# Optimization experiments

Hardware: AMD Instinct MI355X
Metric: run time of the kernel (lower is better)

The kernel has to match this reference:

```python
import jax, jax.numpy as jnp
import numpy as np

B, D, T, H, K = 16, 1024, 1024, 1024, 2  # batch, in_channels, seq_len, hidden_size, kernel_size


def setup_inputs() -> dict:
    key = jax.random.key(0)
    k1, k2, k3 = jax.random.split(key, 3)
    inputs = jax.random.normal(k1, (B, D, T), dtype=jnp.float32)
    # Conv1D kernel in OIH layout: [3H, D, K]; scaled to keep gates in a sane range
    conv_w = jax.random.normal(k2, (3 * H, D, K), dtype=jnp.float32) / np.float32(np.sqrt(D * K))
    conv_b = jax.random.normal(k3, (3 * H,), dtype=jnp.float32) * 0.01
    return {"inputs": inputs, "conv_w": conv_w, "conv_b": conv_b}


def reference(inputs, conv_w, conv_b):
    # inputs: [B, D, T] (channels_first, as in the keras call signature)
    # Causal conv: left-pad time by K-1, then VALID conv -> [B, 3H, T]
    padded = jnp.pad(inputs, ((0, 0), (0, 0), (K - 1, 0)))
    gates = jax.lax.conv_general_dilated(
        padded, conv_w, window_strides=(1,), padding="VALID",
        dimension_numbers=("NCH", "OIH", "NCH"))
    gates = gates + conv_b[None, :, None]
    gates = jnp.transpose(gates, (0, 2, 1))  # [B, T, 3H]
    z = jnp.tanh(gates[..., :H])
    f = jax.nn.sigmoid(gates[..., H:2 * H])
    o = jax.nn.sigmoid(gates[..., 2 * H:])

    # fo-pooling linear recurrence: c_t = f_t * c_{t-1} + (1 - f_t) * z_t, c_0 = 0
    zf = (jnp.transpose(z, (1, 0, 2)), jnp.transpose(f, (1, 0, 2)))  # time-major [T, B, H]

    def step(c, zf_t):
        z_t, f_t = zf_t
        c_new = f_t * c + (1.0 - f_t) * z_t
        return c_new, c_new

    c0 = jnp.zeros((B, H), dtype=inputs.dtype)
    _, c_seq = jax.lax.scan(step, c0, zf)
    c_seq = jnp.transpose(c_seq, (1, 0, 2))  # [B, T, H]
    h_seq = o * c_seq
    return c_seq, h_seq
```

## Files before the change

### kernel.cpp

```cpp
#include <hip/hip_runtime.h>

#define Bsz 16
#define Dch 1024
#define Tsz 1024
#define Hsz 1024
#define Mtot (Bsz*Tsz)
#define K2   (2*Dch)
#define Ntot (3*Hsz)
#define NCH  32
#define CL   32
#define NT   32

typedef __attribute__((ext_vector_type(8))) short bf16x8;
typedef __attribute__((ext_vector_type(4))) float f32x4;

__device__ __forceinline__ unsigned short f2bf(float x) {
    unsigned u = __float_as_uint(x);
    u += 0x7FFFu + ((u >> 16) & 1u);
    return (unsigned short)(u >> 16);
}
__device__ __forceinline__ float bf2f(unsigned short s) {
    return __uint_as_float(((unsigned)s) << 16);
}

#define GLOAD_LDS16(gp, lp) \
    __builtin_amdgcn_global_load_lds((const __attribute__((address_space(1))) void*)(gp), \
                                     (__attribute__((address_space(3))) void*)(lp), 16, 0, 0)

#define LDSB(p) ((unsigned)(unsigned long long)(__attribute__((address_space(3))) const void*)(p))

#define DSR(dst, addr, off) \
    asm volatile("ds_read_b128 %0, %1 offset:" #off : "=v"(dst) : "v"(addr))

#define WAITLG(n) do { \
    asm volatile("s_waitcnt lgkmcnt(" #n ")" ::: "memory"); \
    __builtin_amdgcn_sched_barrier(0); } while (0)

#define VMC(n) do { \
    asm volatile("s_waitcnt vmcnt(" #n ")" ::: "memory"); \
    __builtin_amdgcn_sched_barrier(0); } while (0)

#define BAR __builtin_amdgcn_s_barrier()

__global__ __launch_bounds__(256)
void prep(const float* __restrict__ x, unsigned short* __restrict__ a2,
          const float* __restrict__ w, unsigned short* __restrict__ wb) {
    __shared__ float Xs[64][66];
    int bid = blockIdx.x;
    int tid = threadIdx.x;
    if (bid >= 4096) {
        int i0 = (bid - 4096) * 256 + tid;
        #pragma unroll
        for (int k = 0; k < 4; k++) {
            int i = i0 + k * (1536 * 256);
            float4 v = ((const float4*)w)[i];
            ushort4 r;
            r.x = f2bf(v.x); r.y = f2bf(v.y); r.z = f2bf(v.z); r.w = f2bf(v.w);
            ((ushort4*)wb)[i] = r;
        }
        return;
    }
    int b   = bid >> 8;
    int tt0 = ((bid >> 4) & 15) << 6;
    int dd0 = (bid & 15) << 6;
    int colt = tid & 63, rowq = tid >> 6;
    const size_t xbase = (size_t)b * (Dch * Tsz);
    #pragma unroll
    for (int r = 0; r < 16; r++) {
        int dd = r * 4 + rowq;
        Xs[dd][1 + colt] = x[xbase + (size_t)(dd0 + dd) * Tsz + tt0 + colt];
    }
    if (tid < 64) {
        Xs[tid][0] = (tt0 == 0) ? 0.f : x[xbase + (size_t)(dd0 + tid) * Tsz + tt0 - 1];
    }
    __syncthreads();
    #pragma unroll
    for (int r = 0; r < 16; r++) {
        int tr = r * 4 + rowq;
        int dc = colt;
        float v0 = Xs[dc][tr];
        float v1 = Xs[dc][tr + 1];
        unsigned pack = (unsigned)f2bf(v0) | ((unsigned)f2bf(v1) << 16);
        int m = (b << 10) + tt0 + tr;
        ((unsigned*)a2)[(size_t)m * (K2 / 2) + dd0 + dc] = pack;
    }
}

#define MF(slot, bset, p) do { \
    _Pragma("unroll") for (int ks_ = 0; ks_ < 2; ++ks_) { \
      _Pragma("unroll") for (int d_ = 0; d_ < 2; ++d_) { \
        _Pragma("unroll") for (int j_ = 0; j_ < 4; ++j_) { \
          acc[2*(p)+d_][j_] = __builtin_amdgcn_mfma_f32_16x16x32_bf16( \
              slot[d_][ks_], bset[ks_][j_], acc[2*(p)+d_][j_], 0, 0, 0); \
        } } } } while (0)

__global__ __launch_bounds__(512, 2)
void gemm_gates(const unsigned short* __restrict__ A, const unsigned short* __restrict__ Bt,
                const float* __restrict__ bias,
                float* __restrict__ zc, float* __restrict__ fh, unsigned short* __restrict__ ob) {
    __shared__ __align__(16) unsigned short As[2][16384];
    __shared__ __align__(16) unsigned short Bs[2][16384];

    int tid  = threadIdx.x;
    int wv   = tid >> 6, lane = tid & 63;
    int wm   = wv >> 2, wn = wv & 3;
    int lm   = lane & 15, q = lane >> 4;

    int bid = blockIdx.x;
    int swz = (bid & 7) * 96 + (bid >> 3);
    int mt = swz / 12, nt = swz % 12;
    int m0 = mt << 8, n0 = nt << 8;

    const unsigned short* Abase = A  + (size_t)m0 * K2;
    const unsigned short* Bbase = Bt + (size_t)n0 * K2;

    int loff   = (wv * 8 + (lane >> 3)) * K2 + (((lane & 7) ^ (lane >> 3)) << 3);
    int ldsoff = wv * 8 * 64;

    int sw  = lm & 7;
    int kc0 = (q ^ sw) << 3;
    int kc1 = ((4 + q) ^ sw) << 3;
    int aoff = (wm * 128 + lm) * 64;
    int boff = (wn * 64 + lm) * 64;

    unsigned asb = LDSB(&As[0][0]);
    unsigned bsb = LDSB(&Bs[0][0]);
    unsigned aA0 = asb + (unsigned)(aoff + kc0) * 2u;
    unsigned aA1 = asb + (unsigned)(aoff + kc1) * 2u;
    unsigned aB0 = bsb + (unsigned)(boff + kc0) * 2u;
    unsigned aB1 = bsb + (unsigned)(boff + kc1) * 2u;

    f32x4 acc[8][4] = {};
    bf16x8 afA[2][2], afB[2][2];
    bf16x8 bfrE[2][4], bfrO[2][4];

#define STAGE_A(t, h) do { \
    const unsigned short* g_ = Abase + (h) * (128 * K2) + (t) * 64 + loff; \
    unsigned short* l_ = &As[(t) & 1][(h) * 8192 + ldsoff]; \
    GLOAD_LDS16(g_, l_); \
    GLOAD_LDS16(g_ + 64 * K2, l_ + 64 * 64); } while (0)
#define STAGE_B(t, h) do { \
    const unsigned short* g_ = Bbase + (h) * (128 * K2) + (t) * 64 + loff; \
    unsigned short* l_ = &Bs[(t) & 1][(h) * 8192 + ldsoff]; \
    GLOAD_LDS16(g_, l_); \
    GLOAD_LDS16(g_ + 64 * K2, l_ + 64 * 64); } while (0)

#define R_AFP(slot, o0, o1, bo) do { \
    DSR(slot[0][0], aA0 + (bo), o0); DSR(slot[0][1], aA1 + (bo), o0); \
    DSR(slot[1][0], aA0 + (bo), o1); DSR(slot[1][1], aA1 + (bo), o1); } while (0)
#define R_BH0(set, bo) do { \
    DSR(set[0][0], aB0 + (bo), 0);    DSR(set[1][0], aB1 + (bo), 0); \
    DSR(set[0][1], aB0 + (bo), 2048); DSR(set[1][1], aB1 + (bo), 2048); } while (0)
#define R_BH1(set, bo) do { \
    DSR(set[0][2], aB0 + (bo), 4096); DSR(set[1][2], aB1 + (bo), 4096); \
    DSR(set[0][3], aB0 + (bo), 6144); DSR(set[1][3], aB1 + (bo), 6144); } while (0)

#define PRIO1 __builtin_amdgcn_s_setprio(1)
#define PRIO0 do { __builtin_amdgcn_s_setprio(0); __builtin_amdgcn_sched_barrier(0); } while (0)

#define PH0(T, CB, BC) do { \
    R_AFP(afB, 4096, 6144, CB); \
    STAGE_A((T) + 1, 1); \
    WAITLG(4); \
    PRIO1; MF(afA, BC, 0); PRIO0; } while (0)
#define PH1(T, CB, NB, BC, BN) do { \
    R_AFP(afA, 8192, 10240, CB); \
    R_BH0(BN, NB); \
    STAGE_A((T) + 1, 0); \
    WAITLG(8); \
    PRIO1; MF(afB, BC, 1); PRIO0; } while (0)
#define PH2(T, CB, NB, BC, BN) do { \
    R_AFP(afB, 12288, 14336, CB); \
    R_BH1(BN, NB); \
    STAGE_B((T) + 2, 1); \
    WAITLG(8); \
    PRIO1; MF(afA, BC, 2); PRIO0; } while (0)
#define PH3(T, NB, BC) do { \
    R_AFP(afA, 0, 2048, NB); \
    STAGE_B((T) + 2, 0); \
    WAITLG(4); \
    PRIO1; MF(afB, BC, 3); PRIO0; } while (0)

    STAGE_A(0, 0); STAGE_A(0, 1); STAGE_B(0, 0); STAGE_B(0, 1);
    STAGE_B(1, 1); STAGE_B(1, 0);
    VMC(4); BAR;
    R_AFP(afA, 0, 2048, 0u);
    R_BH0(bfrE, 0u); R_BH1(bfrE, 0u);
    __builtin_amdgcn_sched_barrier(0);

    #pragma unroll 1
    for (int tp = 0; tp < 15; ++tp) {
        int t0 = 2 * tp;
        PH0(t0, 0u, bfrE);                 VMC(2); BAR;
        PH1(t0, 0u, 32768u, bfrE, bfrO);           BAR;
        PH2(t0, 0u, 32768u, bfrE, bfrO);   VMC(2); BAR;
        PH3(t0, 32768u, bfrE);                     BAR;
        PH0(t0 + 1, 32768u, bfrO);         VMC(2); BAR;
        PH1(t0 + 1, 32768u, 0u, bfrO, bfrE);       BAR;
        PH2(t0 + 1, 32768u, 0u, bfrO, bfrE); VMC(2); BAR;
        PH3(t0 + 1, 0u, bfrO);                     BAR;
    }

    PH0(30, 0u, bfrE);                     VMC(2); BAR;
    PH1(30, 0u, 32768u, bfrE, bfrO);               BAR;
    R_AFP(afB, 12288, 14336, 0u);
    R_BH1(bfrO, 32768u);
    WAITLG(8);
    PRIO1; MF(afA, bfrE, 2); PRIO0;
    VMC(0); BAR;
    R_AFP(afA, 0, 2048, 32768u);
    WAITLG(4);
    PRIO1; MF(afB, bfrE, 3); PRIO0;
    BAR;

    R_AFP(afB, 4096, 6144, 32768u);
    WAITLG(4);
    PRIO1; MF(afA, bfrO, 0); PRIO0; BAR;
    R_AFP(afA, 8192, 10240, 32768u);
    WAITLG(4);
    PRIO1; MF(afB, bfrO, 1); PRIO0; BAR;
    R_AFP(afB, 12288, 14336, 32768u);
    WAITLG(4);
    PRIO1; MF(afA, bfrO, 2); PRIO0; BAR;
    WAITLG(0);
    PRIO1; MF(afB, bfrO, 3); PRIO0;

    int gt = nt >> 2;
    #pragma unroll
    for (int i = 0; i < 8; ++i) {
        int mrow = m0 + wm * 128 + i * 16 + q * 4;
        #pragma unroll
        for (int j = 0; j < 4; ++j) {
            int n = n0 + wn * 64 + j * 16 + lm;
            float bv = bias[n];
            int hcol = n & 1023;
            #pragma unroll
            for (int r = 0; r < 4; ++r) {
                float g = acc[i][j][r] + bv;
                size_t idx = (size_t)(mrow + r) * Hsz + hcol;
                if (gt == 0) {
                    float e = __expf(2.f * g);
                    zc[idx] = __fdividef(e - 1.f, e + 1.f);
                } else {
                    float s = __fdividef(1.f, 1.f + __expf(-g));
                    if (gt == 1) fh[idx] = s;
                    else         ob[idx] = f2bf(s);
                }
            }
        }
    }
}

__global__ __launch_bounds__(256)
void scan1(const float* __restrict__ zc, const float* __restrict__ fh,
           float* __restrict__ Aw, float* __restrict__ Bw) {
    int blk = blockIdx.x;
    int hb = blk & 1, ch = (blk >> 1) & 31, b = blk >> 6;
    int h = hb * 512 + threadIdx.x * 2;
    size_t base = ((size_t)b << 20) + ((size_t)(ch * CL) << 10) + h;
    float ax = 1.f, ay = 1.f, bx = 0.f, by = 0.f;
    #pragma unroll 8
    for (int s = 0; s < CL; s++) {
        size_t idx = base + ((size_t)s << 10);
        float2 z = *(const float2*)&zc[idx];
        float2 f = *(const float2*)&fh[idx];
        ax *= f.x; ay *= f.y;
        bx = z.x + f.x * (bx - z.x);
        by = z.y + f.y * (by - z.y);
    }
    int o = (ch * Bsz + b) * Hsz + h;
    *(float2*)&Aw[o] = make_float2(ax, ay);
    *(float2*)&Bw[o] = make_float2(bx, by);
}

__global__ __launch_bounds__(256)
void scan3(float* __restrict__ zc, float* __restrict__ fh,
           const unsigned short* __restrict__ ob,
           const float* __restrict__ Aw, const float* __restrict__ Bw) {
    int blk = blockIdx.x;
    int hb = blk & 1, ch = (blk >> 1) & 31, b = blk >> 6;
    int h = hb * 512 + threadIdx.x * 2;
    float cx = 0.f, cy = 0.f;
    for (int cp = 0; cp < ch; cp++) {
        int o = (cp * Bsz + b) * Hsz + h;
        float2 A = *(const float2*)&Aw[o];
        float2 B = *(const float2*)&Bw[o];
        cx = A.x * cx + B.x;
        cy = A.y * cy + B.y;
    }
    size_t base = ((size_t)b << 20) + ((size_t)(ch * CL) << 10) + h;
    #pragma unroll 8
    for (int s = 0; s < CL; s++) {
        size_t idx = base + ((size_t)s << 10);
        float2 z = *(const float2*)&zc[idx];
        float2 f = *(const float2*)&fh[idx];
        unsigned ov = *(const unsigned*)&ob[idx];
        cx = z.x + f.x * (cx - z.x);
        cy = z.y + f.y * (cy - z.y);
        *(float2*)&zc[idx] = make_float2(cx, cy);
        float ox = bf2f((unsigned short)(ov & 0xFFFF));
        float oy = bf2f((unsigned short)(ov >> 16));
        *(float2*)&fh[idx] = make_float2(ox * cx, oy * cy);
    }
}

extern "C" void kernel_launch(void* const* d_in, const int* in_sizes, int n_in,
                              void* d_out, int out_size, void* d_ws, size_t ws_size,
                              hipStream_t stream) {
    const float* x    = (const float*)d_in[0];
    const float* w    = (const float*)d_in[1];
    const float* bias = (const float*)d_in[2];
    float* zc = (float*)d_out;
    float* fh = (float*)d_out + (size_t)Mtot * Hsz;
    unsigned short* a2 = (unsigned short*)d_ws;
    unsigned short* wb = a2 + (size_t)Mtot * K2;
    unsigned short* ob = wb + (size_t)Ntot * K2;
    float* Aw = (float*)(ob + (size_t)Mtot * Hsz);
    float* Bw = Aw + NCH * Bsz * Hsz;

    hipLaunchKernelGGL(prep, dim3(5632), dim3(256), 0, stream, x, a2, w, wb);
    hipLaunchKernelGGL(gemm_gates, dim3(768), dim3(512), 0, stream, a2, wb, bias, zc, fh, ob);
    hipLaunchKernelGGL(scan1, dim3(1024), dim3(256), 0, stream, zc, fh, Aw, Bw);
    hipLaunchKernelGGL(scan3, dim3(1024), dim3(256), 0, stream, zc, fh, ob, Aw, Bw);
}
```

Measured before the change: 453.8 us.

## Restructure GEMM pipeline to stage full tiles once per iteration with fewer barriers

```diff
diff --git a/kernel.cpp b/kernel.cpp
--- a/kernel.cpp
+++ b/kernel.cpp
@@ -158,72 +158,56 @@
 #define PRIO1 __builtin_amdgcn_s_setprio(1)
 #define PRIO0 do { __builtin_amdgcn_s_setprio(0); __builtin_amdgcn_sched_barrier(0); } while (0)
 
-#define PH0(T, CB, BC) do { \
+#define PH012(CB, BC) do { \
     R_AFP(afB, 4096, 6144, CB); \
-    STAGE_A((T) + 1, 1); \
     WAITLG(4); \
-    PRIO1; MF(afA, BC, 0); PRIO0; } while (0)
-#define PH1(T, CB, NB, BC, BN) do { \
+    PRIO1; MF(afA, BC, 0); PRIO0; \
     R_AFP(afA, 8192, 10240, CB); \
-    R_BH0(BN, NB); \
-    STAGE_A((T) + 1, 0); \
-    WAITLG(8); \
-    PRIO1; MF(afB, BC, 1); PRIO0; } while (0)
-#define PH2(T, CB, NB, BC, BN) do { \
+    WAITLG(4); \
+    PRIO1; MF(afB, BC, 1); PRIO0; \
     R_AFP(afB, 12288, 14336, CB); \
-    R_BH1(BN, NB); \
-    STAGE_B((T) + 2, 1); \
-    WAITLG(8); \
-    PRIO1; MF(afA, BC, 2); PRIO0; } while (0)
-#define PH3(T, NB, BC) do { \
+    WAITLG(0); \
+    PRIO1; MF(afA, BC, 2); PRIO0; \
+    VMC(0); \
+    BAR; } while (0)
+
+#define PH3(T, NB, BC, BN) do { \
     R_AFP(afA, 0, 2048, NB); \
-    STAGE_B((T) + 2, 0); \
-    WAITLG(4); \
+    R_BH0(BN, NB); R_BH1(BN, NB); \
+    STAGE_A((T) + 2, 0); STAGE_A((T) + 2, 1); \
+    STAGE_B((T) + 2, 0); STAGE_B((T) + 2, 1); \
+    WAITLG(12); \
     PRIO1; MF(afB, BC, 3); PRIO0; } while (0)
 
+#define PH3_NOSTAGE(NB, BC, BN) do { \
+    R_AFP(afA, 0, 2048, NB); \
+    R_BH0(BN, NB); R_BH1(BN, NB); \
+    WAITLG(12); \
+    PRIO1; MF(afB, BC, 3); PRIO0; } while (0)
+
+#define PH3_LAST(BC) do { \
+    WAITLG(0); \
+    PRIO1; MF(afB, BC, 3); PRIO0; } while (0)
+
     STAGE_A(0, 0); STAGE_A(0, 1); STAGE_B(0, 0); STAGE_B(0, 1);
-    STAGE_B(1, 1); STAGE_B(1, 0);
-    VMC(4); BAR;
+    VMC(0); BAR;
     R_AFP(afA, 0, 2048, 0u);
     R_BH0(bfrE, 0u); R_BH1(bfrE, 0u);
+    STAGE_A(1, 0); STAGE_A(1, 1); STAGE_B(1, 0); STAGE_B(1, 1);
     __builtin_amdgcn_sched_barrier(0);
 
     #pragma unroll 1
     for (int tp = 0; tp < 15; ++tp) {
         int t0 = 2 * tp;
-        PH0(t0, 0u, bfrE);                 VMC(2); BAR;
-        PH1(t0, 0u, 32768u, bfrE, bfrO);           BAR;
-        PH2(t0, 0u, 32768u, bfrE, bfrO);   VMC(2); BAR;
-        PH3(t0, 32768u, bfrE);                     BAR;
-        PH0(t0 + 1, 32768u, bfrO);         VMC(2); BAR;
-        PH1(t0 + 1, 32768u, 0u, bfrO, bfrE);       BAR;
-        PH2(t0 + 1, 32768u, 0u, bfrO, bfrE); VMC(2); BAR;
-        PH3(t0 + 1, 0u, bfrO);                     BAR;
-    }
-
-    PH0(30, 0u, bfrE);                     VMC(2); BAR;
-    PH1(30, 0u, 32768u, bfrE, bfrO);               BAR;
-    R_AFP(afB, 12288, 14336, 0u);
-    R_BH1(bfrO, 32768u);
-    WAITLG(8);
-    PRIO1; MF(afA, bfrE, 2); PRIO0;
-    VMC(0); BAR;
-    R_AFP(afA, 0, 2048, 32768u);
-    WAITLG(4);
-    PRIO1; MF(afB, bfrE, 3); PRIO0;
-    BAR;
-
-    R_AFP(afB, 4096, 6144, 32768u);
-    WAITLG(4);
-    PRIO1; MF(afA, bfrO, 0); PRIO0; BAR;
-    R_AFP(afA, 8192, 10240, 32768u);
-    WAITLG(4);
-    PRIO1; MF(afB, bfrO, 1); PRIO0; BAR;
-    R_AFP(afB, 12288, 14336, 32768u);
-    WAITLG(4);
-    PRIO1; MF(afA, bfrO, 2); PRIO0; BAR;
-    WAITLG(0);
-    PRIO1; MF(afB, bfrO, 3); PRIO0;
+        PH012(0u, bfrE);
+        PH3(t0, 32768u, bfrE, bfrO);
+        PH012(32768u, bfrO);
+        PH3(t0 + 1, 0u, bfrO, bfrE);
+    }
+    PH012(0u, bfrE);
+    PH3_NOSTAGE(32768u, bfrE, bfrO);
+    PH012(32768u, bfrO);
+    PH3_LAST(bfrO);
 
     int gt = nt >> 2;
     #pragma unroll
```

New measurement: 455.8 us. No clear change (+0.4%).
